# Performance work log

Measured on AMD Instinct MI355X. Metric: run time of the kernel, lower is better.

The kernel has to match this reference:

```python
import jax, jax.numpy as jnp
import numpy as np

NUM_CLASSES = 14
TAU = 1.0
LOSS_WEIGHT = 1.0
KERNEL_SUM = 26.0  # 3x3x3 ones with center zeroed


def setup_inputs() -> dict:
    key = jax.random.key(0)
    k1, k2, k3 = jax.random.split(key, 3)
    B, C, H, W, D = 2, NUM_CLASSES, 96, 96, 96
    preds_S = jax.random.normal(k1, (B, C, H, W, D), dtype=jnp.float32)
    preds_T = jax.random.normal(k2, (B, C, H, W, D), dtype=jnp.float32)
    gt_labels = jax.random.randint(k3, (B, 1, H, W, D), 0, NUM_CLASSES).astype(jnp.int32)
    return {"preds_S": preds_S, "preds_T": preds_T, "gt_labels": gt_labels}


def _boundary_masks(gt_labels, num_classes):
    # gt_labels: [B,1,H,W,D] int -> boundary mask [B,K,H,W,D] bool
    B, _, H, W, D = gt_labels.shape
    onehot = (gt_labels == jnp.arange(num_classes, dtype=gt_labels.dtype)[None, :, None, None, None]).astype(jnp.float32)  # [B,K,H,W,D]
    kernel = jnp.ones((1, 1, 3, 3, 3), jnp.float32).at[0, 0, 1, 1, 1].set(0.0)
    x = onehot.reshape(B * num_classes, 1, H, W, D)
    conv = jax.lax.conv_general_dilated(x, kernel, (1, 1, 1), 'SAME')  # [B*K,1,H,W,D]
    conv = conv.reshape(B, num_classes, H, W, D)
    # boundary[boundary == kernel.sum()] = 0; boundary[boundary > 0] = 1
    return (conv > 0.0) & (conv != KERNEL_SUM)


def reference(preds_S, preds_T, gt_labels):
    B, C, H, W, D = preds_S.shape
    V = H * W * D
    # softmax over class dim is per-voxel, identical before/after the gather
    logS = jax.nn.log_softmax(preds_S / TAU, axis=1).reshape(B, C, V)
    logT = jax.nn.log_softmax(preds_T / TAU, axis=1).reshape(B, C, V)
    pT = jnp.exp(logT)
    kl_per_voxel = jnp.sum(pT * (logT - logS), axis=1)  # [B,V] (sum over classes)

    mask = _boundary_masks(gt_labels, NUM_CLASSES).reshape(B, NUM_CLASSES, V).astype(jnp.float32)
    n_b = jnp.sum(mask, axis=-1)                                  # [B,K] boundary voxel counts
    masked_sum = jnp.einsum('bkv,bv->bk', mask, kl_per_voxel)     # [B,K]
    # F.kl_div reduction='mean' averages over all C * n_b elements
    per_cls = jnp.where(n_b > 0, masked_sum / (C * jnp.maximum(n_b, 1.0)), 0.0)
    valid = (n_b > 0).astype(jnp.float32)
    n_valid = jnp.sum(valid)
    loss = jnp.where(n_valid > 0, jnp.sum(per_cls) / jnp.maximum(n_valid, 1.0), 0.0)
    return LOSS_WEIGHT * loss
```

## Files before the change

kernel.cpp:

```cpp
#include <hip/hip_runtime.h>

#define NC 14
#define DIM 96
#define VOL (96 * 96 * 96)
#define VPT 4
#define TPB 256
#define VPB (VPT * TPB)
#define NBPB (VOL / VPB)

__global__ __launch_bounds__(256, 2) void bkd_main(const float* __restrict__ S,
                                                   const float* __restrict__ T,
                                                   const int* __restrict__ L,
                                                   float* __restrict__ partials) {
    const int b = blockIdx.x / NBPB;
    const int local = blockIdx.x % NBPB;
    const int tid = threadIdx.x;
    const int v0 = local * VPB + tid * VPT;
    const int d0 = v0 % DIM;
    const int w = (v0 / DIM) % DIM;
    const int h = v0 / (DIM * DIM);

    const float* Sb = S + (size_t)b * NC * VOL + v0;
    const float* Tb = T + (size_t)b * NC * VOL + v0;
    const int* lab = L + b * VOL;

    const bool has_lo = (d0 > 0);
    const bool has_hi = (d0 + VPT < DIM);
    int4 q[9];
    int plo[9], phi[9];
    bool cvalid[9];
#pragma unroll
    for (int dh = -1; dh <= 1; ++dh) {
#pragma unroll
        for (int dw = -1; dw <= 1; ++dw) {
            const int ci = (dh + 1) * 3 + (dw + 1);
            const int h2 = h + dh, w2 = w + dw;
            const bool ok = ((unsigned)h2 < DIM) & ((unsigned)w2 < DIM);
            cvalid[ci] = ok;
            const int* p = lab + (h2 * DIM + w2) * DIM + d0;
            if (ok) {
                q[ci] = *(const int4*)p;
                plo[ci] = has_lo ? p[-1] : 0;
                phi[ci] = has_hi ? p[4] : 0;
            }
        }
    }

    float4 sv[NC], tv[NC];
#pragma unroll
    for (int c = 0; c < NC; ++c) {
        sv[c] = *(const float4*)(Sb + c * VOL);
        tv[c] = *(const float4*)(Tb + c * VOL);
    }

    __builtin_amdgcn_sched_barrier(0);

    unsigned vmask[VPT] = {0u, 0u, 0u, 0u};
#pragma unroll
    for (int ci = 0; ci < 9; ++ci) {
        if (cvalid[ci]) {
            const unsigned m1 = 1u << q[ci].x;
            const unsigned m2 = 1u << q[ci].y;
            const unsigned m3 = 1u << q[ci].z;
            const unsigned m4 = 1u << q[ci].w;
            const unsigned m0 = has_lo ? (1u << plo[ci]) : 0u;
            const unsigned m5 = has_hi ? (1u << phi[ci]) : 0u;
            const bool isC = (ci == 4);
            vmask[0] |= m0 | m2 | (isC ? 0u : m1);
            vmask[1] |= m1 | m3 | (isC ? 0u : m2);
            vmask[2] |= m2 | m4 | (isC ? 0u : m3);
            vmask[3] |= m3 | m5 | (isC ? 0u : m4);
        }
    }
    {
        const int nh = 3 - (h == 0) - (h == DIM - 1);
        const int nw = 3 - (w == 0) - (w == DIM - 1);
        const int ncols = nh * nw;
        const int nn0 = ncols * (has_lo ? 3 : 2) - 1;
        const int nn12 = ncols * 3 - 1;
        const int nn3 = ncols * (has_hi ? 3 : 2) - 1;
        if (nn0 == 26 && __popc(vmask[0]) == 1) vmask[0] = 0u;
        if (nn12 == 26 && __popc(vmask[1]) == 1) vmask[1] = 0u;
        if (nn12 == 26 && __popc(vmask[2]) == 1) vmask[2] = 0u;
        if (nn3 == 26 && __popc(vmask[3]) == 1) vmask[3] = 0u;
    }

    float ES[VPT] = {0.f, 0.f, 0.f, 0.f};
    float ET[VPT] = {0.f, 0.f, 0.f, 0.f};
    float Aa[VPT] = {0.f, 0.f, 0.f, 0.f};
#pragma unroll
    for (int c = 0; c < NC; ++c) {
        const float4 s = sv[c];
        const float4 t = tv[c];
        { const float es = __expf(s.x), et = __expf(t.x);
          ES[0] += es; ET[0] += et; Aa[0] += et * (t.x - s.x); }
        { const float es = __expf(s.y), et = __expf(t.y);
          ES[1] += es; ET[1] += et; Aa[1] += et * (t.y - s.y); }
        { const float es = __expf(s.z), et = __expf(t.z);
          ES[2] += es; ET[2] += et; Aa[2] += et * (t.z - s.z); }
        { const float es = __expf(s.w), et = __expf(t.w);
          ES[3] += es; ET[3] += et; Aa[3] += et * (t.w - s.w); }
    }

    float kl[VPT];
#pragma unroll
    for (int i = 0; i < VPT; ++i) {
        kl[i] = Aa[i] / ET[i] + __logf(ES[i]) - __logf(ET[i]);
    }

    float acc_sum[NC];
    float acc_cnt[NC];
#pragma unroll
    for (int k = 0; k < NC; ++k) { acc_sum[k] = 0.f; acc_cnt[k] = 0.f; }
#pragma unroll
    for (int i = 0; i < VPT; ++i) {
#pragma unroll
        for (int k = 0; k < NC; ++k) {
            if (vmask[i] & (1u << k)) { acc_sum[k] += kl[i]; acc_cnt[k] += 1.f; }
        }
    }

    __shared__ float lds[4][2 * NC];
    const int lane = tid & 63, wid = tid >> 6;
#pragma unroll
    for (int k = 0; k < NC; ++k) {
        float svv = acc_sum[k], cvv = acc_cnt[k];
#pragma unroll
        for (int off = 32; off; off >>= 1) {
            svv += __shfl_xor(svv, off);
            cvv += __shfl_xor(cvv, off);
        }
        if (lane == 0) { lds[wid][k] = svv; lds[wid][NC + k] = cvv; }
    }
    __syncthreads();
    if (tid < 2 * NC) {
        const float r = lds[0][tid] + lds[1][tid] + lds[2][tid] + lds[3][tid];
        const int k = (tid < NC) ? tid : (tid - NC);
        const int p = (tid < NC) ? (b * NC + k) : (2 * NC + b * NC + k);
        partials[p * NBPB + local] = r;
    }
}

__global__ __launch_bounds__(64) void bkd_reduce(const float* __restrict__ partials,
                                                 float* __restrict__ res) {
    const int p = blockIdx.x;
    const int lane = threadIdx.x;
    float acc = 0.f;
    for (int i = lane; i < NBPB; i += 64) acc += partials[p * NBPB + i];
#pragma unroll
    for (int off = 32; off; off >>= 1) acc += __shfl_xor(acc, off);
    if (lane == 0) res[p] = acc;
}

__global__ __launch_bounds__(64) void bkd_last(const float* __restrict__ res,
                                               float* __restrict__ out) {
    const int j = threadIdx.x;
    float per = 0.f, valid = 0.f;
    if (j < 2 * NC) {
        const float nb = res[2 * NC + j];
        if (nb > 0.f) {
            per = res[j] / (NC * nb);
            valid = 1.f;
        }
    }
#pragma unroll
    for (int off = 32; off; off >>= 1) {
        per += __shfl_xor(per, off);
        valid += __shfl_xor(valid, off);
    }
    if (j == 0) out[0] = (valid > 0.f) ? (per / valid) : 0.f;
}

extern "C" void kernel_launch(void* const* d_in, const int* in_sizes, int n_in,
                              void* d_out, int out_size, void* d_ws, size_t ws_size,
                              hipStream_t stream) {
    const float* S = (const float*)d_in[0];
    const float* T = (const float*)d_in[1];
    const int* L = (const int*)d_in[2];
    float* out = (float*)d_out;
    float* partials = (float*)d_ws;
    float* res = partials + 2 * NC * 2 * NBPB;

    bkd_main<<<dim3(2 * NBPB), dim3(TPB), 0, stream>>>(S, T, L, partials);
    bkd_reduce<<<dim3(4 * NC), dim3(64), 0, stream>>>(partials, res);
    bkd_last<<<dim3(1), dim3(64), 0, stream>>>(res, out);
}
```

Before: 52.45 us.

## Process two voxel tiles per block and merge final reduction kernels

Each main block now loops over two consecutive voxel tiles, which halves the grid size and the number of per-block partial writes and warp reductions. The two tail kernels (per-row reduce and final loss) are merged into one single-block kernel that reduces the partials in shared memory and computes the loss, saving a kernel launch. The trade-off is fewer blocks in flight to hide memory latency, and a serial single-block tail reading twice fewer partials.

```diff
diff --git a/kernel.cpp b/kernel.cpp
--- a/kernel.cpp
+++ b/kernel.cpp
@@ -7,116 +7,120 @@
 #define TPB 256
 #define VPB (VPT * TPB)
 #define NBPB (VOL / VPB)
+#define ITERS 2
+#define NBT (NBPB / ITERS)
 
 __global__ __launch_bounds__(256, 2) void bkd_main(const float* __restrict__ S,
                                                    const float* __restrict__ T,
                                                    const int* __restrict__ L,
                                                    float* __restrict__ partials) {
-    const int b = blockIdx.x / NBPB;
-    const int local = blockIdx.x % NBPB;
+    const int b = blockIdx.x / NBT;
+    const int local = blockIdx.x % NBT;
     const int tid = threadIdx.x;
-    const int v0 = local * VPB + tid * VPT;
-    const int d0 = v0 % DIM;
-    const int w = (v0 / DIM) % DIM;
-    const int h = v0 / (DIM * DIM);
 
-    const float* Sb = S + (size_t)b * NC * VOL + v0;
-    const float* Tb = T + (size_t)b * NC * VOL + v0;
+    const float* Sbase = S + (size_t)b * NC * VOL;
+    const float* Tbase = T + (size_t)b * NC * VOL;
     const int* lab = L + b * VOL;
-
-    const bool has_lo = (d0 > 0);
-    const bool has_hi = (d0 + VPT < DIM);
-    int4 q[9];
-    int plo[9], phi[9];
-    bool cvalid[9];
-#pragma unroll
-    for (int dh = -1; dh <= 1; ++dh) {
-#pragma unroll
-        for (int dw = -1; dw <= 1; ++dw) {
-            const int ci = (dh + 1) * 3 + (dw + 1);
-            const int h2 = h + dh, w2 = w + dw;
-            const bool ok = ((unsigned)h2 < DIM) & ((unsigned)w2 < DIM);
-            cvalid[ci] = ok;
-            const int* p = lab + (h2 * DIM + w2) * DIM + d0;
-            if (ok) {
-                q[ci] = *(const int4*)p;
-                plo[ci] = has_lo ? p[-1] : 0;
-                phi[ci] = has_hi ? p[4] : 0;
-            }
-        }
-    }
-
-    float4 sv[NC], tv[NC];
-#pragma unroll
-    for (int c = 0; c < NC; ++c) {
-        sv[c] = *(const float4*)(Sb + c * VOL);
-        tv[c] = *(const float4*)(Tb + c * VOL);
-    }
-
-    __builtin_amdgcn_sched_barrier(0);
-
-    unsigned vmask[VPT] = {0u, 0u, 0u, 0u};
-#pragma unroll
-    for (int ci = 0; ci < 9; ++ci) {
-        if (cvalid[ci]) {
-            const unsigned m1 = 1u << q[ci].x;
-            const unsigned m2 = 1u << q[ci].y;
-            const unsigned m3 = 1u << q[ci].z;
-            const unsigned m4 = 1u << q[ci].w;
-            const unsigned m0 = has_lo ? (1u << plo[ci]) : 0u;
-            const unsigned m5 = has_hi ? (1u << phi[ci]) : 0u;
-            const bool isC = (ci == 4);
-            vmask[0] |= m0 | m2 | (isC ? 0u : m1);
-            vmask[1] |= m1 | m3 | (isC ? 0u : m2);
-            vmask[2] |= m2 | m4 | (isC ? 0u : m3);
-            vmask[3] |= m3 | m5 | (isC ? 0u : m4);
-        }
-    }
-    {
-        const int nh = 3 - (h == 0) - (h == DIM - 1);
-        const int nw = 3 - (w == 0) - (w == DIM - 1);
-        const int ncols = nh * nw;
-        const int nn0 = ncols * (has_lo ? 3 : 2) - 1;
-        const int nn12 = ncols * 3 - 1;
-        const int nn3 = ncols * (has_hi ? 3 : 2) - 1;
-        if (nn0 == 26 && __popc(vmask[0]) == 1) vmask[0] = 0u;
-        if (nn12 == 26 && __popc(vmask[1]) == 1) vmask[1] = 0u;
-        if (nn12 == 26 && __popc(vmask[2]) == 1) vmask[2] = 0u;
-        if (nn3 == 26 && __popc(vmask[3]) == 1) vmask[3] = 0u;
-    }
-
-    float ES[VPT] = {0.f, 0.f, 0.f, 0.f};
-    float ET[VPT] = {0.f, 0.f, 0.f, 0.f};
-    float Aa[VPT] = {0.f, 0.f, 0.f, 0.f};
-#pragma unroll
-    for (int c = 0; c < NC; ++c) {
-        const float4 s = sv[c];
-        const float4 t = tv[c];
-        { const float es = __expf(s.x), et = __expf(t.x);
-          ES[0] += es; ET[0] += et; Aa[0] += et * (t.x - s.x); }
-        { const float es = __expf(s.y), et = __expf(t.y);
-          ES[1] += es; ET[1] += et; Aa[1] += et * (t.y - s.y); }
-        { const float es = __expf(s.z), et = __expf(t.z);
-          ES[2] += es; ET[2] += et; Aa[2] += et * (t.z - s.z); }
-        { const float es = __expf(s.w), et = __expf(t.w);
-          ES[3] += es; ET[3] += et; Aa[3] += et * (t.w - s.w); }
-    }
-
-    float kl[VPT];
-#pragma unroll
-    for (int i = 0; i < VPT; ++i) {
-        kl[i] = Aa[i] / ET[i] + __logf(ES[i]) - __logf(ET[i]);
-    }
 
     float acc_sum[NC];
     float acc_cnt[NC];
 #pragma unroll
     for (int k = 0; k < NC; ++k) { acc_sum[k] = 0.f; acc_cnt[k] = 0.f; }
+
+#pragma unroll 1
+    for (int it = 0; it < ITERS; ++it) {
+        const int v0 = (local * ITERS + it) * VPB + tid * VPT;
+        const int d0 = v0 % DIM;
+        const int w = (v0 / DIM) % DIM;
+        const int h = v0 / (DIM * DIM);
+        const bool has_lo = (d0 > 0);
+        const bool has_hi = (d0 + VPT < DIM);
+
+        int4 q[9];
+        int plo[9], phi[9];
+        bool cvalid[9];
 #pragma unroll
-    for (int i = 0; i < VPT; ++i) {
+        for (int dh = -1; dh <= 1; ++dh) {
 #pragma unroll
-        for (int k = 0; k < NC; ++k) {
-            if (vmask[i] & (1u << k)) { acc_sum[k] += kl[i]; acc_cnt[k] += 1.f; }
+            for (int dw = -1; dw <= 1; ++dw) {
+                const int ci = (dh + 1) * 3 + (dw + 1);
+                const int h2 = h + dh, w2 = w + dw;
+                const bool ok = ((unsigned)h2 < DIM) & ((unsigned)w2 < DIM);
+                cvalid[ci] = ok;
+                const int* p = lab + (h2 * DIM + w2) * DIM + d0;
+                if (ok) {
+                    q[ci] = *(const int4*)p;
+                    plo[ci] = has_lo ? p[-1] : 0;
+                    phi[ci] = has_hi ? p[4] : 0;
+                }
+            }
+        }
+
+        const float* Sb = Sbase + v0;
+        const float* Tb = Tbase + v0;
+        float4 sv[NC], tv[NC];
+#pragma unroll
+        for (int c = 0; c < NC; ++c) {
+            sv[c] = *(const float4*)(Sb + c * VOL);
+            tv[c] = *(const float4*)(Tb + c * VOL);
+        }
+
+        __builtin_amdgcn_sched_barrier(0);
+
+        unsigned vmask[VPT] = {0u, 0u, 0u, 0u};
+#pragma unroll
+        for (int ci = 0; ci < 9; ++ci) {
+            if (cvalid[ci]) {
+                const unsigned m1 = 1u << q[ci].x;
+                const unsigned m2 = 1u << q[ci].y;
+                const unsigned m3 = 1u << q[ci].z;
+                const unsigned m4 = 1u << q[ci].w;
+                const unsigned m0 = has_lo ? (1u << plo[ci]) : 0u;
+                const unsigned m5 = has_hi ? (1u << phi[ci]) : 0u;
+                const bool isC = (ci == 4);
+                vmask[0] |= m0 | m2 | (isC ? 0u : m1);
+                vmask[1] |= m1 | m3 | (isC ? 0u : m2);
+                vmask[2] |= m2 | m4 | (isC ? 0u : m3);
+                vmask[3] |= m3 | m5 | (isC ? 0u : m4);
+            }
+        }
+        {
+            const int nh = 3 - (h == 0) - (h == DIM - 1);
+            const int nw = 3 - (w == 0) - (w == DIM - 1);
+            const int ncols = nh * nw;
+            const int nn0 = ncols * (has_lo ? 3 : 2) - 1;
+            const int nn12 = ncols * 3 - 1;
+            const int nn3 = ncols * (has_hi ? 3 : 2) - 1;
+            if (nn0 == 26 && __popc(vmask[0]) == 1) vmask[0] = 0u;
+            if (nn12 == 26 && __popc(vmask[1]) == 1) vmask[1] = 0u;
+            if (nn12 == 26 && __popc(vmask[2]) == 1) vmask[2] = 0u;
+            if (nn3 == 26 && __popc(vmask[3]) == 1) vmask[3] = 0u;
+        }
+
+        float ES[VPT] = {0.f, 0.f, 0.f, 0.f};
+        float ET[VPT] = {0.f, 0.f, 0.f, 0.f};
+        float Aa[VPT] = {0.f, 0.f, 0.f, 0.f};
+#pragma unroll
+        for (int c = 0; c < NC; ++c) {
+            const float4 s = sv[c];
+            const float4 t = tv[c];
+            { const float es = __expf(s.x), et = __expf(t.x);
+              ES[0] += es; ET[0] += et; Aa[0] += et * (t.x - s.x); }
+            { const float es = __expf(s.y), et = __expf(t.y);
+              ES[1] += es; ET[1] += et; Aa[1] += et * (t.y - s.y); }
+            { const float es = __expf(s.z), et = __expf(t.z);
+              ES[2] += es; ET[2] += et; Aa[2] += et * (t.z - s.z); }
+            { const float es = __expf(s.w), et = __expf(t.w);
+              ES[3] += es; ET[3] += et; Aa[3] += et * (t.w - s.w); }
+        }
+
+#pragma unroll
+        for (int i = 0; i < VPT; ++i) {
+            const float kl = Aa[i] / ET[i] + __logf(ES[i]) - __logf(ET[i]);
+#pragma unroll
+            for (int k = 0; k < NC; ++k) {
+                if (vmask[i] & (1u << k)) { acc_sum[k] += kl; acc_cnt[k] += 1.f; }
+            }
         }
     }
 
@@ -137,38 +141,40 @@
         const float r = lds[0][tid] + lds[1][tid] + lds[2][tid] + lds[3][tid];
         const int k = (tid < NC) ? tid : (tid - NC);
         const int p = (tid < NC) ? (b * NC + k) : (2 * NC + b * NC + k);
-        partials[p * NBPB + local] = r;
+        partials[p * NBT + local] = r;
     }
 }
 
-__global__ __launch_bounds__(64) void bkd_reduce(const float* __restrict__ partials,
-                                                 float* __restrict__ res) {
-    const int p = blockIdx.x;
-    const int lane = threadIdx.x;
-    float acc = 0.f;
-    for (int i = lane; i < NBPB; i += 64) acc += partials[p * NBPB + i];
+__global__ __launch_bounds__(256) void bkd_tail(const float* __restrict__ partials,
+                                                float* __restrict__ out) {
+    __shared__ float res[4 * NC];
+    const int tid = threadIdx.x;
+    if (tid < 224) {
+        const int row = tid >> 2, sub = tid & 3;
+        float acc = 0.f;
+        for (int i = sub; i < NBT; i += 4) acc += partials[row * NBT + i];
+        acc += __shfl_xor(acc, 1);
+        acc += __shfl_xor(acc, 2);
+        if (sub == 0) res[row] = acc;
+    }
+    __syncthreads();
+    if (tid < 64) {
+        float per = 0.f, valid = 0.f;
+        if (tid < 2 * NC && tid < NC + NC) {  }
+        if (tid < 28) {
+            const float nb = res[28 + tid];
+            if (nb > 0.f) {
+                per = res[tid] / (NC * nb);
+                valid = 1.f;
+            }
+        }
 #pragma unroll
-    for (int off = 32; off; off >>= 1) acc += __shfl_xor(acc, off);
-    if (lane == 0) res[p] = acc;
-}
-
-__global__ __launch_bounds__(64) void bkd_last(const float* __restrict__ res,
-                                               float* __restrict__ out) {
-    const int j = threadIdx.x;
-    float per = 0.f, valid = 0.f;
-    if (j < 2 * NC) {
-        const float nb = res[2 * NC + j];
-        if (nb > 0.f) {
-            per = res[j] / (NC * nb);
-            valid = 1.f;
+        for (int off = 32; off; off >>= 1) {
+            per += __shfl_xor(per, off);
+            valid += __shfl_xor(valid, off);
         }
+        if (tid == 0) out[0] = (valid > 0.f) ? (per / valid) : 0.f;
     }
-#pragma unroll
-    for (int off = 32; off; off >>= 1) {
-        per += __shfl_xor(per, off);
-        valid += __shfl_xor(valid, off);
-    }
-    if (j == 0) out[0] = (valid > 0.f) ? (per / valid) : 0.f;
 }
 
 extern "C" void kernel_launch(void* const* d_in, const int* in_sizes, int n_in,
@@ -179,9 +185,7 @@
     const int* L = (const int*)d_in[2];
     float* out = (float*)d_out;
     float* partials = (float*)d_ws;
-    float* res = partials + 2 * NC * 2 * NBPB;
 
-    bkd_main<<<dim3(2 * NBPB), dim3(TPB), 0, stream>>>(S, T, L, partials);
-    bkd_reduce<<<dim3(4 * NC), dim3(64), 0, stream>>>(partials, res);
-    bkd_last<<<dim3(1), dim3(64), 0, stream>>>(res, out);
+    bkd_main<<<dim3(2 * NBT), dim3(TPB), 0, stream>>>(S, T, L, partials);
+    bkd_tail<<<dim3(1), dim3(256), 0, stream>>>(partials, out);
 }
```

After: 62.16 us. 18.5% more time.
